# Performance work log

Hardware: AMD Instinct MI355X
Metric: run time of the kernel (lower is better)

The kernel has to match this reference:

```python
import jax, jax.numpy as jnp
import numpy as np

NUM_GRAPHS = 4096


def setup_inputs() -> dict:
    key = jax.random.key(0)
    k1, k2, k3, k4 = jax.random.split(key, 4)
    N, H = 500000, 256
    x = jax.random.normal(k1, (N, H), dtype=jnp.float32)
    batch = jnp.sort(jax.random.randint(k2, (N,), 0, NUM_GRAPHS, dtype=jnp.int64))
    W1 = jax.random.normal(k3, (H, H), dtype=jnp.float32) * (1.0 / np.sqrt(H))
    b1 = jnp.zeros((H,), dtype=jnp.float32)
    w2 = jax.random.normal(k4, (H, 1), dtype=jnp.float32) * (1.0 / np.sqrt(H))
    return {"x": x, "batch": batch, "W1": W1, "b1": b1, "w2": w2}


def reference(x, batch, W1, b1, w2):
    # attention scores: Linear -> Tanh -> Linear(no bias)  -> [N, 1]
    scores = jnp.tanh(x @ W1 + b1) @ w2  # [N, 1]
    # Torch code scatter-maxes into a zeros buffer, so the effective per-graph
    # max is clamped below at 0 (faithfully replicated here).
    seg_max = jax.ops.segment_max(scores, batch, num_segments=NUM_GRAPHS)  # [G, 1]
    seg_max = jnp.maximum(seg_max, 0.0)
    exp_scores = jnp.exp(scores - seg_max[batch])  # [N, 1]
    sum_exp = jax.ops.segment_sum(exp_scores, batch, num_segments=NUM_GRAPHS)  # [G, 1]
    normalized = exp_scores / sum_exp[batch]  # [N, 1]
    graph_embedding = jax.ops.segment_sum(x * normalized, batch, num_segments=NUM_GRAPHS)  # [G, H]
    return graph_embedding
```

## Files before the change

kernel.cpp:

```cpp
#include <hip/hip_runtime.h>
#include <cstdint>

#define H 256
#define MT 64

typedef _Float16 half8 __attribute__((ext_vector_type(8)));
typedef float floatx4 __attribute__((ext_vector_type(4)));

__device__ __forceinline__ float fast_tanh(float v) {
    v = fminf(fmaxf(v, -15.f), 15.f);
    float e = __expf(2.f * v);
    return (e - 1.f) / (e + 1.f);
}

__global__ void setup_kernel(const float* __restrict__ W1,
                             float4* __restrict__ out4, float* __restrict__ Z,
                             _Float16* __restrict__ w1c, int total4, int G) {
    int i = blockIdx.x * 256 + threadIdx.x;
    if (i < total4) out4[i] = make_float4(0.f, 0.f, 0.f, 0.f);
    if (i < G) Z[i] = 0.f;
    if (i < H * H) {
        int r = i & 511;
        int lane = r >> 3, h = r & 7;
        int t = i >> 9;
        int kc = t & 1, s = (t >> 1) & 3, ct = t >> 3;
        int mm = lane & 15, qq = lane >> 4;
        int col = ct * 16 + mm;
        int k = s * 64 + kc * 32 + qq * 8 + h;
        w1c[i] = (_Float16)W1[k * H + col];
    }
}

__global__ __launch_bounds__(256, 3) void fused_kernel(
    const float* __restrict__ x, const _Float16* __restrict__ w1c,
    const float* __restrict__ b1, const float* __restrict__ w2,
    const int* __restrict__ batch,
    float* __restrict__ out, float* __restrict__ Z, int N) {
    __shared__ _Float16 As[2][64][64];
    __shared__ float sred[4][64];
    __shared__ float sexp[64];
    __shared__ int gid[64];

    const int tid = threadIdx.x;
    const int wv = tid >> 6;
    const int lane = tid & 63;
    const int m = lane & 15;
    const int q = lane >> 4;
    const int row0 = blockIdx.x * MT;

    const int srow = tid >> 2;
    const int sc4 = tid & 3;
    const int sg0 = (sc4 * 2) ^ (srow & 7);
    const int sg1 = (sc4 * 2 + 1) ^ (srow & 7);
    const bool srok = (row0 + srow) < N;
    const float* sbase = x + (size_t)(row0 + srow) * H + sc4 * 16;

    floatx4 acc[4][4] = {};

    float4 f0, f1, f2, f3;
    f0 = f1 = f2 = f3 = make_float4(0.f, 0.f, 0.f, 0.f);
    if (srok) {
        const float4* p = (const float4*)sbase;
        f0 = p[0]; f1 = p[1]; f2 = p[2]; f3 = p[3];
    }
    {
        half8 h0, h1;
        h0[0] = (_Float16)f0.x; h0[1] = (_Float16)f0.y; h0[2] = (_Float16)f0.z; h0[3] = (_Float16)f0.w;
        h0[4] = (_Float16)f1.x; h0[5] = (_Float16)f1.y; h0[6] = (_Float16)f1.z; h0[7] = (_Float16)f1.w;
        h1[0] = (_Float16)f2.x; h1[1] = (_Float16)f2.y; h1[2] = (_Float16)f2.z; h1[3] = (_Float16)f2.w;
        h1[4] = (_Float16)f3.x; h1[5] = (_Float16)f3.y; h1[6] = (_Float16)f3.z; h1[7] = (_Float16)f3.w;
        *(half8*)&As[0][srow][sg0 * 8] = h0;
        *(half8*)&As[0][srow][sg1 * 8] = h1;
    }
    __syncthreads();

    for (int s = 0; s < 4; ++s) {
        const int cur = s & 1;
        if (s < 3 && srok) {
            const float4* p = (const float4*)(sbase + (s + 1) * 64);
            f0 = p[0]; f1 = p[1]; f2 = p[2]; f3 = p[3];
        }
        half8 bf[4][2];
#pragma unroll
        for (int ni = 0; ni < 4; ++ni) {
            int ct = wv * 4 + ni;
#pragma unroll
            for (int kc = 0; kc < 2; ++kc) {
                int chunk = ((ct << 2) | s) * 2 + kc;
                bf[ni][kc] = *(const half8*)(w1c + ((size_t)chunk << 9) + lane * 8);
            }
        }
        half8 af[4][2];
#pragma unroll
        for (int mi = 0; mi < 4; ++mi) {
            int r = mi * 16 + m;
#pragma unroll
            for (int kc = 0; kc < 2; ++kc) {
                int g = (kc * 4 + q) ^ (r & 7);
                af[mi][kc] = *(const half8*)&As[cur][r][g * 8];
            }
        }
#pragma unroll
        for (int mi = 0; mi < 4; ++mi)
#pragma unroll
            for (int ni = 0; ni < 4; ++ni) {
                acc[mi][ni] = __builtin_amdgcn_mfma_f32_16x16x32_f16(
                    af[mi][0], bf[ni][0], acc[mi][ni], 0, 0, 0);
                acc[mi][ni] = __builtin_amdgcn_mfma_f32_16x16x32_f16(
                    af[mi][1], bf[ni][1], acc[mi][ni], 0, 0, 0);
            }
        if (s < 3) {
            half8 h0, h1;
            h0[0] = (_Float16)f0.x; h0[1] = (_Float16)f0.y; h0[2] = (_Float16)f0.z; h0[3] = (_Float16)f0.w;
            h0[4] = (_Float16)f1.x; h0[5] = (_Float16)f1.y; h0[6] = (_Float16)f1.z; h0[7] = (_Float16)f1.w;
            h1[0] = (_Float16)f2.x; h1[1] = (_Float16)f2.y; h1[2] = (_Float16)f2.z; h1[3] = (_Float16)f2.w;
            h1[4] = (_Float16)f3.x; h1[5] = (_Float16)f3.y; h1[6] = (_Float16)f3.z; h1[7] = (_Float16)f3.w;
            *(half8*)&As[1 - cur][srow][sg0 * 8] = h0;
            *(half8*)&As[1 - cur][srow][sg1 * 8] = h1;
        }
        __syncthreads();
    }

    float b1c[4], w2c[4];
#pragma unroll
    for (int ni = 0; ni < 4; ++ni) {
        int c = wv * 64 + ni * 16 + m;
        b1c[ni] = b1[c];
        w2c[ni] = w2[c];
    }
#pragma unroll
    for (int mi = 0; mi < 4; ++mi) {
#pragma unroll
        for (int r = 0; r < 4; ++r) {
            float v = 0.f;
#pragma unroll
            for (int ni = 0; ni < 4; ++ni)
                v += w2c[ni] * fast_tanh(acc[mi][ni][r] + b1c[ni]);
            v += __shfl_xor(v, 1);
            v += __shfl_xor(v, 2);
            v += __shfl_xor(v, 4);
            v += __shfl_xor(v, 8);
            if (m == 0) sred[wv][mi * 16 + q * 4 + r] = v;
        }
    }
    __syncthreads();
    if (tid < MT) {
        int row = row0 + tid;
        if (row < N) {
            float sc = sred[0][tid] + sred[1][tid] + sred[2][tid] + sred[3][tid];
            sexp[tid] = __expf(sc);
            gid[tid] = batch[row];
        } else {
            sexp[tid] = 0.f;
            gid[tid] = batch[N - 1];
        }
    }
    __syncthreads();

    const int nval = min(MT, N - row0);
    const float* px = x + (size_t)row0 * H + tid;
    float acc2 = 0.f, zacc = 0.f;
    int cur = gid[0];
#pragma unroll 4
    for (int r = 0; r < nval; ++r) {
        int g = gid[r];
        float w = sexp[r];
        float xv = px[(size_t)r * H];
        if (g != cur) {
            atomicAdd(&out[(size_t)cur * H + tid], acc2);
            if (tid == 0) atomicAdd(&Z[cur], zacc);
            acc2 = 0.f; zacc = 0.f; cur = g;
        }
        acc2 = fmaf(w, xv, acc2);
        zacc += w;
    }
    atomicAdd(&out[(size_t)cur * H + tid], acc2);
    if (tid == 0) atomicAdd(&Z[cur], zacc);
}

__global__ void normalize_kernel(float4* __restrict__ out4,
                                 const float* __restrict__ Z, int total4) {
    int i = blockIdx.x * 256 + threadIdx.x;
    if (i < total4) {
        float s = Z[i >> 6];
        if (s > 0.f) {
            float inv = 1.f / s;
            float4 v = out4[i];
            v.x *= inv; v.y *= inv; v.z *= inv; v.w *= inv;
            out4[i] = v;
        } else {
            out4[i] = make_float4(0.f, 0.f, 0.f, 0.f);
        }
    }
}

extern "C" void kernel_launch(void* const* d_in, const int* in_sizes, int n_in,
                              void* d_out, int out_size, void* d_ws, size_t ws_size,
                              hipStream_t stream) {
    const float* x = (const float*)d_in[0];
    const int* batch = (const int*)d_in[1];
    const float* W1 = (const float*)d_in[2];
    const float* b1 = (const float*)d_in[3];
    const float* w2 = (const float*)d_in[4];
    float* out = (float*)d_out;

    const int N = in_sizes[0] / H;
    const int G = out_size / H;

    char* ws = (char*)d_ws;
    float* Z = (float*)ws;
    size_t off = (size_t)G * sizeof(float);
    off = (off + 15) & ~(size_t)15;
    _Float16* w1c = (_Float16*)(ws + off);

    const int total4 = (G * H) / 4;
    int setup_items = max(total4, H * H);
    setup_kernel<<<(setup_items + 255) / 256, 256, 0, stream>>>(
        W1, (float4*)out, Z, w1c, total4, G);
    fused_kernel<<<(N + MT - 1) / MT, 256, 0, stream>>>(
        x, w1c, b1, w2, batch, out, Z, N);
    normalize_kernel<<<(total4 + 255) / 256, 256, 0, stream>>>(
        (float4*)out, Z, total4);
}
```

Measured before the change: 823.1 us.

## Split fused kernel into score pass and atomic-free per-segment reduction

Replaces the single fused kernel, which used atomics into a zeroed output plus a separate normalize pass, with three stages. A setup kernel builds segment start offsets from the sorted batch array. A score kernel writes exp(score) per row, using a single full-K LDS tile instead of double buffering and folding the bias into the accumulator init. A segment kernel then has one wave per graph reduce its rows and normalize in place. This removes atomics and the normalize launch, but reads x a second time from memory. Per-wave segment work is also unbalanced when graph sizes differ.

```diff
diff --git a/kernel.cpp b/kernel.cpp
--- a/kernel.cpp
+++ b/kernel.cpp
@@ -14,32 +14,38 @@
 }
 
 __global__ void setup_kernel(const float* __restrict__ W1,
-                             float4* __restrict__ out4, float* __restrict__ Z,
-                             _Float16* __restrict__ w1c, int total4, int G) {
-    int i = blockIdx.x * 256 + threadIdx.x;
-    if (i < total4) out4[i] = make_float4(0.f, 0.f, 0.f, 0.f);
-    if (i < G) Z[i] = 0.f;
-    if (i < H * H) {
-        int r = i & 511;
-        int lane = r >> 3, h = r & 7;
-        int t = i >> 9;
-        int kc = t & 1, s = (t >> 1) & 3, ct = t >> 3;
-        int mm = lane & 15, qq = lane >> 4;
-        int col = ct * 16 + mm;
-        int k = s * 64 + kc * 32 + qq * 8 + h;
-        w1c[i] = (_Float16)W1[k * H + col];
-    }
-}
-
-__global__ __launch_bounds__(256, 3) void fused_kernel(
+                             _Float16* __restrict__ w1c,
+                             const int* __restrict__ batch,
+                             int* __restrict__ start, int N, int G,
+                             int total) {
+    for (int i = blockIdx.x * 256 + threadIdx.x; i < total;
+         i += gridDim.x * 256) {
+        if (i < H * H) {
+            int r = i & 511;
+            int lane = r >> 3, h = r & 7;
+            int t = i >> 9;
+            int kc = t & 1, s = (t >> 1) & 3, ct = t >> 3;
+            int mm = lane & 15, qq = lane >> 4;
+            int col = ct * 16 + mm;
+            int k = s * 64 + kc * 32 + qq * 8 + h;
+            w1c[i] = (_Float16)W1[k * H + col];
+        }
+        if (i < N) {
+            int b = batch[i];
+            int prev = (i > 0) ? batch[i - 1] : -1;
+            for (int g = prev + 1; g <= b; ++g) start[g] = i;
+            if (i == N - 1)
+                for (int g = b + 1; g <= G; ++g) start[g] = N;
+        }
+    }
+}
+
+__global__ __launch_bounds__(256, 3) void score_kernel(
     const float* __restrict__ x, const _Float16* __restrict__ w1c,
     const float* __restrict__ b1, const float* __restrict__ w2,
-    const int* __restrict__ batch,
-    float* __restrict__ out, float* __restrict__ Z, int N) {
-    __shared__ _Float16 As[2][64][64];
+    float* __restrict__ wexp, int N) {
+    __shared__ _Float16 As[64][256];
     __shared__ float sred[4][64];
-    __shared__ float sexp[64];
-    __shared__ int gid[64];
 
     const int tid = threadIdx.x;
     const int wv = tid >> 6;
@@ -50,36 +56,47 @@
 
     const int srow = tid >> 2;
     const int sc4 = tid & 3;
+    const bool srok = (row0 + srow) < N;
+    const float* sbase = x + (size_t)(row0 + srow) * H + sc4 * 16;
     const int sg0 = (sc4 * 2) ^ (srow & 7);
     const int sg1 = (sc4 * 2 + 1) ^ (srow & 7);
-    const bool srok = (row0 + srow) < N;
-    const float* sbase = x + (size_t)(row0 + srow) * H + sc4 * 16;
-
-    floatx4 acc[4][4] = {};
-
-    float4 f0, f1, f2, f3;
-    f0 = f1 = f2 = f3 = make_float4(0.f, 0.f, 0.f, 0.f);
+
+    float b1c[4], w2c[4];
+#pragma unroll
+    for (int ni = 0; ni < 4; ++ni) {
+        int c = wv * 64 + ni * 16 + m;
+        b1c[ni] = b1[c];
+        w2c[ni] = w2[c];
+    }
+
     if (srok) {
-        const float4* p = (const float4*)sbase;
-        f0 = p[0]; f1 = p[1]; f2 = p[2]; f3 = p[3];
-    }
-    {
-        half8 h0, h1;
-        h0[0] = (_Float16)f0.x; h0[1] = (_Float16)f0.y; h0[2] = (_Float16)f0.z; h0[3] = (_Float16)f0.w;
-        h0[4] = (_Float16)f1.x; h0[5] = (_Float16)f1.y; h0[6] = (_Float16)f1.z; h0[7] = (_Float16)f1.w;
-        h1[0] = (_Float16)f2.x; h1[1] = (_Float16)f2.y; h1[2] = (_Float16)f2.z; h1[3] = (_Float16)f2.w;
-        h1[4] = (_Float16)f3.x; h1[5] = (_Float16)f3.y; h1[6] = (_Float16)f3.z; h1[7] = (_Float16)f3.w;
-        *(half8*)&As[0][srow][sg0 * 8] = h0;
-        *(half8*)&As[0][srow][sg1 * 8] = h1;
-    }
+#pragma unroll
+        for (int s = 0; s < 4; ++s) {
+            const float4* p = (const float4*)(sbase + s * 64);
+            float4 f0 = p[0], f1 = p[1], f2 = p[2], f3 = p[3];
+            half8 h0, h1;
+            h0[0] = (_Float16)f0.x; h0[1] = (_Float16)f0.y; h0[2] = (_Float16)f0.z; h0[3] = (_Float16)f0.w;
+            h0[4] = (_Float16)f1.x; h0[5] = (_Float16)f1.y; h0[6] = (_Float16)f1.z; h0[7] = (_Float16)f1.w;
+            h1[0] = (_Float16)f2.x; h1[1] = (_Float16)f2.y; h1[2] = (_Float16)f2.z; h1[3] = (_Float16)f2.w;
+            h1[4] = (_Float16)f3.x; h1[5] = (_Float16)f3.y; h1[6] = (_Float16)f3.z; h1[7] = (_Float16)f3.w;
+            *(half8*)&As[srow][s * 64 + sg0 * 8] = h0;
+            *(half8*)&As[srow][s * 64 + sg1 * 8] = h1;
+        }
+    }
+
+    floatx4 acc[4][4];
+#pragma unroll
+    for (int mi = 0; mi < 4; ++mi)
+#pragma unroll
+        for (int ni = 0; ni < 4; ++ni) {
+            floatx4 v;
+            v[0] = b1c[ni]; v[1] = b1c[ni]; v[2] = b1c[ni]; v[3] = b1c[ni];
+            acc[mi][ni] = v;
+        }
+
     __syncthreads();
 
     for (int s = 0; s < 4; ++s) {
-        const int cur = s & 1;
-        if (s < 3 && srok) {
-            const float4* p = (const float4*)(sbase + (s + 1) * 64);
-            f0 = p[0]; f1 = p[1]; f2 = p[2]; f3 = p[3];
-        }
         half8 bf[4][2];
 #pragma unroll
         for (int ni = 0; ni < 4; ++ni) {
@@ -97,7 +114,7 @@
 #pragma unroll
             for (int kc = 0; kc < 2; ++kc) {
                 int g = (kc * 4 + q) ^ (r & 7);
-                af[mi][kc] = *(const half8*)&As[cur][r][g * 8];
+                af[mi][kc] = *(const half8*)&As[r][s * 64 + g * 8];
             }
         }
 #pragma unroll
@@ -109,25 +126,8 @@
                 acc[mi][ni] = __builtin_amdgcn_mfma_f32_16x16x32_f16(
                     af[mi][1], bf[ni][1], acc[mi][ni], 0, 0, 0);
             }
-        if (s < 3) {
-            half8 h0, h1;
-            h0[0] = (_Float16)f0.x; h0[1] = (_Float16)f0.y; h0[2] = (_Float16)f0.z; h0[3] = (_Float16)f0.w;
-            h0[4] = (_Float16)f1.x; h0[5] = (_Float16)f1.y; h0[6] = (_Float16)f1.z; h0[7] = (_Float16)f1.w;
-            h1[0] = (_Float16)f2.x; h1[1] = (_Float16)f2.y; h1[2] = (_Float16)f2.z; h1[3] = (_Float16)f2.w;
-            h1[4] = (_Float16)f3.x; h1[5] = (_Float16)f3.y; h1[6] = (_Float16)f3.z; h1[7] = (_Float16)f3.w;
-            *(half8*)&As[1 - cur][srow][sg0 * 8] = h0;
-            *(half8*)&As[1 - cur][srow][sg1 * 8] = h1;
-        }
-        __syncthreads();
-    }
-
-    float b1c[4], w2c[4];
-#pragma unroll
-    for (int ni = 0; ni < 4; ++ni) {
-        int c = wv * 64 + ni * 16 + m;
-        b1c[ni] = b1[c];
-        w2c[ni] = w2[c];
-    }
+    }
+
 #pragma unroll
     for (int mi = 0; mi < 4; ++mi) {
 #pragma unroll
@@ -135,7 +135,7 @@
             float v = 0.f;
 #pragma unroll
             for (int ni = 0; ni < 4; ++ni)
-                v += w2c[ni] * fast_tanh(acc[mi][ni][r] + b1c[ni]);
+                v += w2c[ni] * fast_tanh(acc[mi][ni][r]);
             v += __shfl_xor(v, 1);
             v += __shfl_xor(v, 2);
             v += __shfl_xor(v, 4);
@@ -148,50 +148,36 @@
         int row = row0 + tid;
         if (row < N) {
             float sc = sred[0][tid] + sred[1][tid] + sred[2][tid] + sred[3][tid];
-            sexp[tid] = __expf(sc);
-            gid[tid] = batch[row];
-        } else {
-            sexp[tid] = 0.f;
-            gid[tid] = batch[N - 1];
-        }
-    }
-    __syncthreads();
-
-    const int nval = min(MT, N - row0);
-    const float* px = x + (size_t)row0 * H + tid;
-    float acc2 = 0.f, zacc = 0.f;
-    int cur = gid[0];
+            wexp[row] = __expf(sc);
+        }
+    }
+}
+
+__global__ __launch_bounds__(256, 4) void seg_kernel(
+    const float* __restrict__ x, const float* __restrict__ wexp,
+    const int* __restrict__ start, float4* __restrict__ out4, int G) {
+    const int wv = threadIdx.x >> 6;
+    const int lane = threadIdx.x & 63;
+    const int g = blockIdx.x * 4 + wv;
+    if (g >= G) return;
+    const int lo = start[g];
+    const int hi = start[g + 1];
+    const float4* px = (const float4*)x + lane;
+    float4 a = make_float4(0.f, 0.f, 0.f, 0.f);
+    float z = 0.f;
 #pragma unroll 4
-    for (int r = 0; r < nval; ++r) {
-        int g = gid[r];
-        float w = sexp[r];
-        float xv = px[(size_t)r * H];
-        if (g != cur) {
-            atomicAdd(&out[(size_t)cur * H + tid], acc2);
-            if (tid == 0) atomicAdd(&Z[cur], zacc);
-            acc2 = 0.f; zacc = 0.f; cur = g;
-        }
-        acc2 = fmaf(w, xv, acc2);
-        zacc += w;
-    }
-    atomicAdd(&out[(size_t)cur * H + tid], acc2);
-    if (tid == 0) atomicAdd(&Z[cur], zacc);
-}
-
-__global__ void normalize_kernel(float4* __restrict__ out4,
-                                 const float* __restrict__ Z, int total4) {
-    int i = blockIdx.x * 256 + threadIdx.x;
-    if (i < total4) {
-        float s = Z[i >> 6];
-        if (s > 0.f) {
-            float inv = 1.f / s;
-            float4 v = out4[i];
-            v.x *= inv; v.y *= inv; v.z *= inv; v.w *= inv;
-            out4[i] = v;
-        } else {
-            out4[i] = make_float4(0.f, 0.f, 0.f, 0.f);
-        }
-    }
+    for (int r = lo; r < hi; ++r) {
+        float w = wexp[r];
+        float4 v = px[(size_t)r * (H / 4)];
+        z += w;
+        a.x = fmaf(w, v.x, a.x);
+        a.y = fmaf(w, v.y, a.y);
+        a.z = fmaf(w, v.z, a.z);
+        a.w = fmaf(w, v.w, a.w);
+    }
+    float inv = (hi > lo) ? 1.f / z : 0.f;
+    a.x *= inv; a.y *= inv; a.z *= inv; a.w *= inv;
+    out4[(size_t)g * (H / 4) + lane] = a;
 }
 
 extern "C" void kernel_launch(void* const* d_in, const int* in_sizes, int n_in,
@@ -208,17 +194,19 @@
     const int G = out_size / H;
 
     char* ws = (char*)d_ws;
-    float* Z = (float*)ws;
-    size_t off = (size_t)G * sizeof(float);
+    _Float16* w1c = (_Float16*)ws;
+    int* start = (int*)(ws + (size_t)H * H * sizeof(_Float16));
+    size_t off = (size_t)H * H * sizeof(_Float16) + (size_t)(G + 1) * sizeof(int);
     off = (off + 15) & ~(size_t)15;
-    _Float16* w1c = (_Float16*)(ws + off);
-
-    const int total4 = (G * H) / 4;
-    int setup_items = max(total4, H * H);
-    setup_kernel<<<(setup_items + 255) / 256, 256, 0, stream>>>(
-        W1, (float4*)out, Z, w1c, total4, G);
-    fused_kernel<<<(N + MT - 1) / MT, 256, 0, stream>>>(
-        x, w1c, b1, w2, batch, out, Z, N);
-    normalize_kernel<<<(total4 + 255) / 256, 256, 0, stream>>>(
-        (float4*)out, Z, total4);
-}
+    float* wexp = (float*)(ws + off);
+
+    int setup_items = (N > H * H) ? N : (H * H);
+    int setup_blocks = (setup_items + 255) / 256;
+    if (setup_blocks > 2048) setup_blocks = 2048;
+    setup_kernel<<<setup_blocks, 256, 0, stream>>>(
+        W1, w1c, batch, start, N, G, setup_items);
+    score_kernel<<<(N + MT - 1) / MT, 256, 0, stream>>>(
+        x, w1c, b1, w2, wexp, N);
+    seg_kernel<<<(G + 3) / 4, 256, 0, stream>>>(
+        x, wexp, start, (float4*)out, G);
+}
```

Result: faster. 797.7 us (-3.1%).

## Make fused kernel persistent with cross-tile prefetch and carried segment accumulators

Applied to the files above, without the earlier changes.

Turns the one-tile-per-block fused kernel into a persistent kernel of 512 blocks, each walking a contiguous range of 64-row tiles. The whole next tile is loaded into registers while the current tile's MFMA, softmax weighting and pooling run, and it is stored into a full-width double-buffered LDS tile afterwards. The running per-graph accumulator now carries across tiles, which cuts the number of atomics at tile boundaries. Bias is folded into the accumulator init. In exchange the kernel uses more registers and LDS (occupancy hint drops from 3 to 2) and has fewer blocks to hide latency.

```diff
diff --git a/kernel.cpp b/kernel.cpp
--- a/kernel.cpp
+++ b/kernel.cpp
@@ -3,6 +3,7 @@
 
 #define H 256
 #define MT 64
+#define PBLOCKS 512
 
 typedef _Float16 half8 __attribute__((ext_vector_type(8)));
 typedef float floatx4 __attribute__((ext_vector_type(4)));
@@ -31,12 +32,12 @@
     }
 }
 
-__global__ __launch_bounds__(256, 3) void fused_kernel(
+__global__ __launch_bounds__(256, 2) void fused_kernel(
     const float* __restrict__ x, const _Float16* __restrict__ w1c,
     const float* __restrict__ b1, const float* __restrict__ w2,
     const int* __restrict__ batch,
-    float* __restrict__ out, float* __restrict__ Z, int N) {
-    __shared__ _Float16 As[2][64][64];
+    float* __restrict__ out, float* __restrict__ Z, int N, int nt, int tpb) {
+    __shared__ _Float16 As[2][64][256];
     __shared__ float sred[4][64];
     __shared__ float sexp[64];
     __shared__ int gid[64];
@@ -46,80 +47,15 @@
     const int lane = tid & 63;
     const int m = lane & 15;
     const int q = lane >> 4;
-    const int row0 = blockIdx.x * MT;
+
+    const int t0 = blockIdx.x * tpb;
+    const int t1 = (t0 + tpb < nt) ? (t0 + tpb) : nt;
+    if (t0 >= nt) return;
 
     const int srow = tid >> 2;
     const int sc4 = tid & 3;
     const int sg0 = (sc4 * 2) ^ (srow & 7);
     const int sg1 = (sc4 * 2 + 1) ^ (srow & 7);
-    const bool srok = (row0 + srow) < N;
-    const float* sbase = x + (size_t)(row0 + srow) * H + sc4 * 16;
-
-    floatx4 acc[4][4] = {};
-
-    float4 f0, f1, f2, f3;
-    f0 = f1 = f2 = f3 = make_float4(0.f, 0.f, 0.f, 0.f);
-    if (srok) {
-        const float4* p = (const float4*)sbase;
-        f0 = p[0]; f1 = p[1]; f2 = p[2]; f3 = p[3];
-    }
-    {
-        half8 h0, h1;
-        h0[0] = (_Float16)f0.x; h0[1] = (_Float16)f0.y; h0[2] = (_Float16)f0.z; h0[3] = (_Float16)f0.w;
-        h0[4] = (_Float16)f1.x; h0[5] = (_Float16)f1.y; h0[6] = (_Float16)f1.z; h0[7] = (_Float16)f1.w;
-        h1[0] = (_Float16)f2.x; h1[1] = (_Float16)f2.y; h1[2] = (_Float16)f2.z; h1[3] = (_Float16)f2.w;
-        h1[4] = (_Float16)f3.x; h1[5] = (_Float16)f3.y; h1[6] = (_Float16)f3.z; h1[7] = (_Float16)f3.w;
-        *(half8*)&As[0][srow][sg0 * 8] = h0;
-        *(half8*)&As[0][srow][sg1 * 8] = h1;
-    }
-    __syncthreads();
-
-    for (int s = 0; s < 4; ++s) {
-        const int cur = s & 1;
-        if (s < 3 && srok) {
-            const float4* p = (const float4*)(sbase + (s + 1) * 64);
-            f0 = p[0]; f1 = p[1]; f2 = p[2]; f3 = p[3];
-        }
-        half8 bf[4][2];
-#pragma unroll
-        for (int ni = 0; ni < 4; ++ni) {
-            int ct = wv * 4 + ni;
-#pragma unroll
-            for (int kc = 0; kc < 2; ++kc) {
-                int chunk = ((ct << 2) | s) * 2 + kc;
-                bf[ni][kc] = *(const half8*)(w1c + ((size_t)chunk << 9) + lane * 8);
-            }
-        }
-        half8 af[4][2];
-#pragma unroll
-        for (int mi = 0; mi < 4; ++mi) {
-            int r = mi * 16 + m;
-#pragma unroll
-            for (int kc = 0; kc < 2; ++kc) {
-                int g = (kc * 4 + q) ^ (r & 7);
-                af[mi][kc] = *(const half8*)&As[cur][r][g * 8];
-            }
-        }
-#pragma unroll
-        for (int mi = 0; mi < 4; ++mi)
-#pragma unroll
-            for (int ni = 0; ni < 4; ++ni) {
-                acc[mi][ni] = __builtin_amdgcn_mfma_f32_16x16x32_f16(
-                    af[mi][0], bf[ni][0], acc[mi][ni], 0, 0, 0);
-                acc[mi][ni] = __builtin_amdgcn_mfma_f32_16x16x32_f16(
-                    af[mi][1], bf[ni][1], acc[mi][ni], 0, 0, 0);
-            }
-        if (s < 3) {
-            half8 h0, h1;
-            h0[0] = (_Float16)f0.x; h0[1] = (_Float16)f0.y; h0[2] = (_Float16)f0.z; h0[3] = (_Float16)f0.w;
-            h0[4] = (_Float16)f1.x; h0[5] = (_Float16)f1.y; h0[6] = (_Float16)f1.z; h0[7] = (_Float16)f1.w;
-            h1[0] = (_Float16)f2.x; h1[1] = (_Float16)f2.y; h1[2] = (_Float16)f2.z; h1[3] = (_Float16)f2.w;
-            h1[4] = (_Float16)f3.x; h1[5] = (_Float16)f3.y; h1[6] = (_Float16)f3.z; h1[7] = (_Float16)f3.w;
-            *(half8*)&As[1 - cur][srow][sg0 * 8] = h0;
-            *(half8*)&As[1 - cur][srow][sg1 * 8] = h1;
-        }
-        __syncthreads();
-    }
 
     float b1c[4], w2c[4];
 #pragma unroll
@@ -128,54 +64,156 @@
         b1c[ni] = b1[c];
         w2c[ni] = w2[c];
     }
-#pragma unroll
-    for (int mi = 0; mi < 4; ++mi) {
-#pragma unroll
-        for (int r = 0; r < 4; ++r) {
-            float v = 0.f;
-#pragma unroll
-            for (int ni = 0; ni < 4; ++ni)
-                v += w2c[ni] * fast_tanh(acc[mi][ni][r] + b1c[ni]);
-            v += __shfl_xor(v, 1);
-            v += __shfl_xor(v, 2);
-            v += __shfl_xor(v, 4);
-            v += __shfl_xor(v, 8);
-            if (m == 0) sred[wv][mi * 16 + q * 4 + r] = v;
-        }
+
+    float4 f[4][4];
+    bool nok;
+
+#define LOAD16(T)                                                          \
+    {                                                                      \
+        const float* sb = x + (size_t)((T) * MT + srow) * H + sc4 * 16;    \
+        _Pragma("unroll") for (int s = 0; s < 4; ++s) {                    \
+            const float4* p = (const float4*)(sb + s * 64);                \
+            f[s][0] = p[0]; f[s][1] = p[1]; f[s][2] = p[2]; f[s][3] = p[3];\
+        }                                                                  \
+    }
+
+#define CVT_STORE(B)                                                       \
+    {                                                                      \
+        _Pragma("unroll") for (int s = 0; s < 4; ++s) {                    \
+            half8 h0, h1;                                                  \
+            h0[0] = (_Float16)f[s][0].x; h0[1] = (_Float16)f[s][0].y;      \
+            h0[2] = (_Float16)f[s][0].z; h0[3] = (_Float16)f[s][0].w;      \
+            h0[4] = (_Float16)f[s][1].x; h0[5] = (_Float16)f[s][1].y;      \
+            h0[6] = (_Float16)f[s][1].z; h0[7] = (_Float16)f[s][1].w;      \
+            h1[0] = (_Float16)f[s][2].x; h1[1] = (_Float16)f[s][2].y;      \
+            h1[2] = (_Float16)f[s][2].z; h1[3] = (_Float16)f[s][2].w;      \
+            h1[4] = (_Float16)f[s][3].x; h1[5] = (_Float16)f[s][3].y;      \
+            h1[6] = (_Float16)f[s][3].z; h1[7] = (_Float16)f[s][3].w;      \
+            *(half8*)&As[B][srow][s * 64 + sg0 * 8] = h0;                  \
+            *(half8*)&As[B][srow][s * 64 + sg1 * 8] = h1;                  \
+        }                                                                  \
+    }
+
+    {
+        bool ok = (t0 * MT + srow) < N;
+        if (ok) { LOAD16(t0); CVT_STORE(0); }
     }
     __syncthreads();
-    if (tid < MT) {
-        int row = row0 + tid;
-        if (row < N) {
-            float sc = sred[0][tid] + sred[1][tid] + sred[2][tid] + sred[3][tid];
-            sexp[tid] = __expf(sc);
-            gid[tid] = batch[row];
-        } else {
-            sexp[tid] = 0.f;
-            gid[tid] = batch[N - 1];
-        }
-    }
-    __syncthreads();
-
-    const int nval = min(MT, N - row0);
-    const float* px = x + (size_t)row0 * H + tid;
+
     float acc2 = 0.f, zacc = 0.f;
-    int cur = gid[0];
-#pragma unroll 4
-    for (int r = 0; r < nval; ++r) {
-        int g = gid[r];
-        float w = sexp[r];
-        float xv = px[(size_t)r * H];
-        if (g != cur) {
-            atomicAdd(&out[(size_t)cur * H + tid], acc2);
-            if (tid == 0) atomicAdd(&Z[cur], zacc);
-            acc2 = 0.f; zacc = 0.f; cur = g;
-        }
-        acc2 = fmaf(w, xv, acc2);
-        zacc += w;
-    }
-    atomicAdd(&out[(size_t)cur * H + tid], acc2);
-    if (tid == 0) atomicAdd(&Z[cur], zacc);
+    int cur = -1;
+
+    for (int t = t0; t < t1; ++t) {
+        const int buf = (t - t0) & 1;
+        const int row0 = t * MT;
+
+        nok = false;
+        if (t + 1 < t1) {
+            nok = ((t + 1) * MT + srow) < N;
+            if (nok) LOAD16(t + 1);
+        }
+
+        floatx4 acc[4][4];
+#pragma unroll
+        for (int mi = 0; mi < 4; ++mi)
+#pragma unroll
+            for (int ni = 0; ni < 4; ++ni) {
+                floatx4 v;
+                v[0] = b1c[ni]; v[1] = b1c[ni]; v[2] = b1c[ni]; v[3] = b1c[ni];
+                acc[mi][ni] = v;
+            }
+
+        for (int s = 0; s < 4; ++s) {
+            half8 bf[4][2];
+#pragma unroll
+            for (int ni = 0; ni < 4; ++ni) {
+                int ct = wv * 4 + ni;
+#pragma unroll
+                for (int kc = 0; kc < 2; ++kc) {
+                    int chunk = ((ct << 2) | s) * 2 + kc;
+                    bf[ni][kc] = *(const half8*)(w1c + ((size_t)chunk << 9) + lane * 8);
+                }
+            }
+            half8 af[4][2];
+#pragma unroll
+            for (int mi = 0; mi < 4; ++mi) {
+                int r = mi * 16 + m;
+#pragma unroll
+                for (int kc = 0; kc < 2; ++kc) {
+                    int g = (kc * 4 + q) ^ (r & 7);
+                    af[mi][kc] = *(const half8*)&As[buf][r][s * 64 + g * 8];
+                }
+            }
+#pragma unroll
+            for (int mi = 0; mi < 4; ++mi)
+#pragma unroll
+                for (int ni = 0; ni < 4; ++ni) {
+                    acc[mi][ni] = __builtin_amdgcn_mfma_f32_16x16x32_f16(
+                        af[mi][0], bf[ni][0], acc[mi][ni], 0, 0, 0);
+                    acc[mi][ni] = __builtin_amdgcn_mfma_f32_16x16x32_f16(
+                        af[mi][1], bf[ni][1], acc[mi][ni], 0, 0, 0);
+                }
+        }
+
+#pragma unroll
+        for (int mi = 0; mi < 4; ++mi) {
+#pragma unroll
+            for (int r = 0; r < 4; ++r) {
+                float v = 0.f;
+#pragma unroll
+                for (int ni = 0; ni < 4; ++ni)
+                    v += w2c[ni] * fast_tanh(acc[mi][ni][r]);
+                v += __shfl_xor(v, 1);
+                v += __shfl_xor(v, 2);
+                v += __shfl_xor(v, 4);
+                v += __shfl_xor(v, 8);
+                if (m == 0) sred[wv][mi * 16 + q * 4 + r] = v;
+            }
+        }
+        __syncthreads();
+        if (tid < MT) {
+            int row = row0 + tid;
+            if (row < N) {
+                float sc = sred[0][tid] + sred[1][tid] + sred[2][tid] + sred[3][tid];
+                sexp[tid] = __expf(sc);
+                gid[tid] = batch[row];
+            } else {
+                sexp[tid] = 0.f;
+                gid[tid] = batch[N - 1];
+            }
+        }
+        __syncthreads();
+
+        {
+            const int nval = (N - row0 < MT) ? (N - row0) : MT;
+            const float* px = x + (size_t)row0 * H + tid;
+#pragma unroll 8
+            for (int r = 0; r < nval; ++r) {
+                int g = gid[r];
+                float w = sexp[r];
+                float xv = px[(size_t)r * H];
+                if (g != cur) {
+                    if (cur >= 0) {
+                        atomicAdd(&out[(size_t)cur * H + tid], acc2);
+                        if (tid == 0) atomicAdd(&Z[cur], zacc);
+                    }
+                    acc2 = 0.f; zacc = 0.f; cur = g;
+                }
+                acc2 = fmaf(w, xv, acc2);
+                zacc += w;
+            }
+        }
+
+        if (t + 1 < t1 && nok) CVT_STORE(buf ^ 1);
+        __syncthreads();
+    }
+
+    if (cur >= 0) {
+        atomicAdd(&out[(size_t)cur * H + tid], acc2);
+        if (tid == 0) atomicAdd(&Z[cur], zacc);
+    }
+#undef LOAD16
+#undef CVT_STORE
 }
 
 __global__ void normalize_kernel(float4* __restrict__ out4,
@@ -214,11 +252,15 @@
     _Float16* w1c = (_Float16*)(ws + off);
 
     const int total4 = (G * H) / 4;
-    int setup_items = max(total4, H * H);
+    int setup_items = (total4 > H * H) ? total4 : (H * H);
     setup_kernel<<<(setup_items + 255) / 256, 256, 0, stream>>>(
         W1, (float4*)out, Z, w1c, total4, G);
-    fused_kernel<<<(N + MT - 1) / MT, 256, 0, stream>>>(
-        x, w1c, b1, w2, batch, out, Z, N);
+
+    const int nt = (N + MT - 1) / MT;
+    const int tpb = (nt + PBLOCKS - 1) / PBLOCKS;
+    fused_kernel<<<PBLOCKS, 256, 0, stream>>>(
+        x, w1c, b1, w2, batch, out, Z, N, nt, tpb);
+
     normalize_kernel<<<(total4 + 255) / 256, 256, 0, stream>>>(
         (float4*)out, Z, total4);
 }
```

After: 1.162 ms. 41.2% more time.
